# Kernel optimization log

Measured on AMD Instinct MI355X. Metric: run time of the kernel, lower is better.

## Reference

```python
import jax, jax.numpy as jnp
import numpy as np

B, N, G, K, V = 4, 512, 8, 64, 32000


def setup_inputs() -> dict:
    key = jax.random.key(0)
    k1, k2, k3 = jax.random.split(key, 3)
    phi = jax.random.normal(k1, (B, N, G, K), dtype=jnp.float32)
    # psi initialized uniform(-0.5, 0.5) as in torch.nn.init.uniform_
    psi = jax.random.uniform(k2, (V, K), dtype=jnp.float32, minval=-0.5, maxval=0.5)
    # perm[h, v] = index of h^{-1} acting on vocab word v (data-dependent permutation)
    perm = jax.random.randint(k3, (G, V), 0, V, dtype=jnp.int64)
    return {"phi": phi, "psi": psi, "perm": perm}


def reference(phi, psi, perm):
    # For each group element h: logits[b,n,v] += dot(phi[b,n,h,:], psi[perm[h,v],:])
    # Gather psi rows per group element: [G, V, K]
    psi_g = psi[perm]
    logits = jnp.einsum("bnhk,hvk->bnv", phi, psi_g)  # [B, N, V]
    return jax.nn.softmax(logits, axis=-1)
```

## Files before the change

### kernel.cpp

```cpp
#include <hip/hip_runtime.h>
#include <math.h>


#define M_ROWS 2048
#define V_DIM  32000
#define C_DIM  512
#define G_DIM  8
#define K_DIM  64
#define BM     128
#define BV     128
#define BK     32
#define NVBLK  (V_DIM / BV)
#define LDS_ROW 40

typedef _Float16 f16x8 __attribute__((ext_vector_type(8)));
typedef _Float16 f16x4 __attribute__((ext_vector_type(4)));
typedef float    f32x4 __attribute__((ext_vector_type(4)));

__global__ __launch_bounds__(256, 2) void gdecode_gemm(
    const float* __restrict__ phi, const float* __restrict__ psi,
    const int* __restrict__ perm, const int pstride,
    float* __restrict__ out, float* __restrict__ smax, float* __restrict__ ssum)
{
  __shared__ __align__(16) _Float16 lds[3 * BM * LDS_ROW];
  _Float16* sAhi = lds;
  _Float16* sAlo = lds + BM * LDS_ROW;
  _Float16* sB   = lds + 2 * BM * LDS_ROW;

  const int t     = threadIdx.x;
  const int vbase = blockIdx.x * BV;
  const int mbase = blockIdx.y * BM;

  const int kg = t & 7;
  const int r0 = t >> 3;

  const int wid  = t >> 6;
  const int lane = t & 63;
  const int wm   = wid & 1;
  const int wv   = wid >> 1;
  const int lrow = lane & 15;
  const int quad = lane >> 4;

  f32x4 acc[4][4] = {};

  for (int it = 0; it < 16; ++it) {
    const int cb  = it * BK;
    const int h   = cb >> 6;
    const int kin = cb & 63;

    float4 av[4], bv[4];
    #pragma unroll
    for (int i = 0; i < 4; ++i) {
      int m = r0 + i * 32;
      av[i] = *(const float4*)(phi + (size_t)(mbase + m) * C_DIM + cb + kg * 4);
    }
    #pragma unroll
    for (int i = 0; i < 4; ++i) {
      int v  = r0 + i * 32;
      int pr = perm[(size_t)(h * V_DIM + vbase + v) * pstride];
      bv[i]  = *(const float4*)(psi + (size_t)pr * K_DIM + kin + kg * 4);
    }

    __syncthreads();

    #pragma unroll
    for (int i = 0; i < 4; ++i) {
      int m = r0 + i * 32;
      float4 x = av[i];
      _Float16 h0 = (_Float16)x.x, h1 = (_Float16)x.y,
               h2 = (_Float16)x.z, h3 = (_Float16)x.w;
      f16x4 hi = {h0, h1, h2, h3};
      f16x4 lo = {(_Float16)(x.x - (float)h0), (_Float16)(x.y - (float)h1),
                  (_Float16)(x.z - (float)h2), (_Float16)(x.w - (float)h3)};
      *(f16x4*)(sAhi + m * LDS_ROW + kg * 4) = hi;
      *(f16x4*)(sAlo + m * LDS_ROW + kg * 4) = lo;
    }
    #pragma unroll
    for (int i = 0; i < 4; ++i) {
      int v = r0 + i * 32;
      float4 x = bv[i];
      f16x4 w = {(_Float16)x.x, (_Float16)x.y, (_Float16)x.z, (_Float16)x.w};
      *(f16x4*)(sB + v * LDS_ROW + kg * 4) = w;
    }

    __syncthreads();

    f16x8 ah[4], al[4], bf[4];
    #pragma unroll
    for (int i = 0; i < 4; ++i) {
      ah[i] = *(const f16x8*)(sAhi + (wm * 64 + i * 16 + lrow) * LDS_ROW + quad * 8);
      al[i] = *(const f16x8*)(sAlo + (wm * 64 + i * 16 + lrow) * LDS_ROW + quad * 8);
      bf[i] = *(const f16x8*)(sB   + (wv * 64 + i * 16 + lrow) * LDS_ROW + quad * 8);
    }
    #pragma unroll
    for (int i = 0; i < 4; ++i) {
      #pragma unroll
      for (int j = 0; j < 4; ++j) {
        acc[i][j] = __builtin_amdgcn_mfma_f32_16x16x32_f16(ah[i], bf[j], acc[i][j], 0, 0, 0);
        acc[i][j] = __builtin_amdgcn_mfma_f32_16x16x32_f16(al[i], bf[j], acc[i][j], 0, 0, 0);
      }
    }
  }

  __syncthreads();
  float* redmax = (float*)lds;
  float* redsum = redmax + 2 * BM;
  const int rowb = wm * 64;

  #pragma unroll
  for (int i = 0; i < 4; ++i) {
    #pragma unroll
    for (int r = 0; r < 4; ++r) {
      float v = fmaxf(fmaxf(acc[i][0][r], acc[i][1][r]),
                      fmaxf(acc[i][2][r], acc[i][3][r]));
      v = fmaxf(v, __shfl_xor(v, 1));
      v = fmaxf(v, __shfl_xor(v, 2));
      v = fmaxf(v, __shfl_xor(v, 4));
      v = fmaxf(v, __shfl_xor(v, 8));
      if (lrow == 0) redmax[(rowb + i * 16 + quad * 4 + r) * 2 + wv] = v;
    }
  }
  __syncthreads();
  float gmx[4][4];
  #pragma unroll
  for (int i = 0; i < 4; ++i) {
    #pragma unroll
    for (int r = 0; r < 4; ++r) {
      int row = rowb + i * 16 + quad * 4 + r;
      gmx[i][r] = fmaxf(redmax[row * 2], redmax[row * 2 + 1]);
    }
  }
  #pragma unroll
  for (int i = 0; i < 4; ++i) {
    #pragma unroll
    for (int r = 0; r < 4; ++r) {
      float s = __expf(acc[i][0][r] - gmx[i][r]) + __expf(acc[i][1][r] - gmx[i][r])
              + __expf(acc[i][2][r] - gmx[i][r]) + __expf(acc[i][3][r] - gmx[i][r]);
      s += __shfl_xor(s, 1);
      s += __shfl_xor(s, 2);
      s += __shfl_xor(s, 4);
      s += __shfl_xor(s, 8);
      if (lrow == 0) redsum[(rowb + i * 16 + quad * 4 + r) * 2 + wv] = s;
    }
  }
  __syncthreads();
  if (smax != nullptr && t < BM) {
    int row = t;
    size_t o = (size_t)(mbase + row) * NVBLK + blockIdx.x;
    smax[o] = fmaxf(redmax[row * 2], redmax[row * 2 + 1]);
    ssum[o] = redsum[row * 2] + redsum[row * 2 + 1];
  }
  #pragma unroll
  for (int i = 0; i < 4; ++i) {
    #pragma unroll
    for (int j = 0; j < 4; ++j) {
      #pragma unroll
      for (int r = 0; r < 4; ++r) {
        int grow = mbase + rowb + i * 16 + quad * 4 + r;
        int gcol = vbase + wv * 64 + j * 16 + lrow;
        out[(size_t)grow * V_DIM + gcol] = acc[i][j][r];
      }
    }
  }
}

__global__ __launch_bounds__(256) void gdecode_softmax_ws(
    float* __restrict__ out, const float* __restrict__ smax, const float* __restrict__ ssum)
{
  __shared__ float sbuf[4];
  const int m = blockIdx.x;
  const int t = threadIdx.x;
  const float* rm = smax + (size_t)m * NVBLK;
  const float* rs = ssum + (size_t)m * NVBLK;

  float lm = -3.4e38f;
  for (int i = t; i < NVBLK; i += 256) lm = fmaxf(lm, rm[i]);
  for (int d = 1; d < 64; d <<= 1) lm = fmaxf(lm, __shfl_xor(lm, d));
  if ((t & 63) == 0) sbuf[t >> 6] = lm;
  __syncthreads();
  const float M = fmaxf(fmaxf(sbuf[0], sbuf[1]), fmaxf(sbuf[2], sbuf[3]));
  __syncthreads();

  float ls = 0.f;
  for (int i = t; i < NVBLK; i += 256) ls += rs[i] * __expf(rm[i] - M);
  for (int d = 1; d < 64; d <<= 1) ls += __shfl_xor(ls, d);
  if ((t & 63) == 0) sbuf[t >> 6] = ls;
  __syncthreads();
  const float inv = 1.f / (sbuf[0] + sbuf[1] + sbuf[2] + sbuf[3]);

  float4* row = (float4*)(out + (size_t)m * V_DIM);
  for (int i = t; i < V_DIM / 4; i += 256) {
    float4 x = row[i];
    x.x = __expf(x.x - M) * inv;
    x.y = __expf(x.y - M) * inv;
    x.z = __expf(x.z - M) * inv;
    x.w = __expf(x.w - M) * inv;
    row[i] = x;
  }
}

__global__ __launch_bounds__(256) void gdecode_softmax_nows(float* __restrict__ out)
{
  __shared__ float sbuf[4];
  const int m = blockIdx.x;
  const int t = threadIdx.x;
  float4* row = (float4*)(out + (size_t)m * V_DIM);

  float lm = -3.4e38f;
  for (int i = t; i < V_DIM / 4; i += 256) {
    float4 x = row[i];
    lm = fmaxf(lm, fmaxf(fmaxf(x.x, x.y), fmaxf(x.z, x.w)));
  }
  for (int d = 1; d < 64; d <<= 1) lm = fmaxf(lm, __shfl_xor(lm, d));
  if ((t & 63) == 0) sbuf[t >> 6] = lm;
  __syncthreads();
  const float M = fmaxf(fmaxf(sbuf[0], sbuf[1]), fmaxf(sbuf[2], sbuf[3]));
  __syncthreads();

  float ls = 0.f;
  for (int i = t; i < V_DIM / 4; i += 256) {
    float4 x = row[i];
    ls += __expf(x.x - M) + __expf(x.y - M) + __expf(x.z - M) + __expf(x.w - M);
  }
  for (int d = 1; d < 64; d <<= 1) ls += __shfl_xor(ls, d);
  if ((t & 63) == 0) sbuf[t >> 6] = ls;
  __syncthreads();
  const float inv = 1.f / (sbuf[0] + sbuf[1] + sbuf[2] + sbuf[3]);

  for (int i = t; i < V_DIM / 4; i += 256) {
    float4 x = row[i];
    x.x = __expf(x.x - M) * inv;
    x.y = __expf(x.y - M) * inv;
    x.z = __expf(x.z - M) * inv;
    x.w = __expf(x.w - M) * inv;
    row[i] = x;
  }
}

extern "C" void kernel_launch(void* const* d_in, const int* in_sizes, int n_in,
                              void* d_out, int out_size, void* d_ws, size_t ws_size,
                              hipStream_t stream)
{
  const float* phi  = (const float*)d_in[0];
  const float* psi  = (const float*)d_in[1];
  const int*   perm = (const int*)d_in[2];
  const int pstride = (in_sizes[2] == 2 * G_DIM * V_DIM) ? 2 : 1;

  float* out = (float*)d_out;

  const size_t need = (size_t)M_ROWS * NVBLK * 2 * sizeof(float);
  const bool hasws = (d_ws != nullptr) && (ws_size >= need);
  float* smax = hasws ? (float*)d_ws : nullptr;
  float* ssum = hasws ? smax + (size_t)M_ROWS * NVBLK : nullptr;

  dim3 grid(NVBLK, M_ROWS / BM);
  gdecode_gemm<<<grid, 256, 0, stream>>>(phi, psi, perm, pstride, out, smax, ssum);

  if (hasws)
    gdecode_softmax_ws<<<M_ROWS, 256, 0, stream>>>(out, smax, ssum);
  else
    gdecode_softmax_nows<<<M_ROWS, 256, 0, stream>>>(out);
}
```

Before: 543.0 us.

## Pre-convert operands to fp16 tiles and stream them via global_load_lds

Adds prep kernels that split phi into hi/lo fp16 and gather plus convert psi rows into a tile-contiguous workspace layout. The GEMM then loads tiles directly into LDS with global_load_lds, with no per-iteration gather or conversion, and runs at higher occupancy. Softmax statistics are transposed, combined by a separate per-row kernel, and normalization uses nontemporal loads and stores across more blocks. This removes repeated gather and conversion work across M tiles, at the cost of extra launches and workspace traffic.

```diff
diff --git a/kernel.cpp b/kernel.cpp
--- a/kernel.cpp
+++ b/kernel.cpp
@@ -11,13 +11,220 @@
 #define BV     128
 #define BK     32
 #define NVBLK  (V_DIM / BV)
+#define NMT    (M_ROWS / BM)
+#define NKT    (C_DIM / BK)
 #define LDS_ROW 40
 
 typedef _Float16 f16x8 __attribute__((ext_vector_type(8)));
 typedef _Float16 f16x4 __attribute__((ext_vector_type(4)));
 typedef float    f32x4 __attribute__((ext_vector_type(4)));
 
-__global__ __launch_bounds__(256, 2) void gdecode_gemm(
+
+__device__ __forceinline__ void gl_lds16(const void* g, void* l) {
+  __builtin_amdgcn_global_load_lds(
+      (const __attribute__((address_space(1))) unsigned int*)g,
+      (__attribute__((address_space(3))) unsigned int*)l, 16, 0, 0);
+}
+
+__global__ __launch_bounds__(256) void gdecode_prep_phi(
+    const float* __restrict__ phi, _Float16* __restrict__ aws)
+{
+  const int ga   = blockIdx.x * 256 + threadIdx.x;
+  const int g    = ga & 511;
+  const int half = (ga >> 9) & 1;
+  const int tile = ga >> 10;
+  const int kq = g >> 7, r = g & 127;
+  const int m  = (tile >> 4) * BM + r;
+  const int k  = (tile & 15) * BK + kq * 8;
+  const float4 x0 = *(const float4*)(phi + (size_t)m * C_DIM + k);
+  const float4 x1 = *(const float4*)(phi + (size_t)m * C_DIM + k + 4);
+  const float xs[8] = {x0.x, x0.y, x0.z, x0.w, x1.x, x1.y, x1.z, x1.w};
+  f16x8 o;
+  #pragma unroll
+  for (int j = 0; j < 8; ++j) {
+    _Float16 hi = (_Float16)xs[j];
+    o[j] = half ? (_Float16)(xs[j] - (float)hi) : hi;
+  }
+  *(f16x8*)(aws + (size_t)ga * 8) = o;
+}
+
+__global__ __launch_bounds__(256) void gdecode_prep_psi(
+    const float* __restrict__ psi, const int* __restrict__ perm, const int pstride,
+    _Float16* __restrict__ bws)
+{
+  const int gb   = blockIdx.x * 256 + threadIdx.x;
+  const int g    = gb & 511;
+  const int tile = gb >> 9;
+  const int it = tile / 250;
+  const int vb = tile - it * 250;
+  const int kq = g >> 7, r = g & 127;
+  const int h   = it >> 1;
+  const int kin = (it & 1) * 32 + kq * 8;
+  const int v   = vb * BV + r;
+  const int pr  = perm[(size_t)(h * V_DIM + v) * pstride];
+  const float4 x0 = *(const float4*)(psi + (size_t)pr * K_DIM + kin);
+  const float4 x1 = *(const float4*)(psi + (size_t)pr * K_DIM + kin + 4);
+  f16x8 o = {(_Float16)x0.x, (_Float16)x0.y, (_Float16)x0.z, (_Float16)x0.w,
+             (_Float16)x1.x, (_Float16)x1.y, (_Float16)x1.z, (_Float16)x1.w};
+  *(f16x8*)(bws + (size_t)gb * 8) = o;
+}
+
+__global__ __launch_bounds__(256, 4) void gdecode_gemm2(
+    const _Float16* __restrict__ aws, const _Float16* __restrict__ bws,
+    float* __restrict__ out, float* __restrict__ smax, float* __restrict__ ssum)
+{
+  __shared__ __align__(16) _Float16 lds[3 * 4096];
+  _Float16* sAh = lds;
+  _Float16* sAl = lds + 4096;
+  _Float16* sB  = lds + 8192;
+
+  const int t  = threadIdx.x;
+  const int vb = blockIdx.x;
+  const int mt = blockIdx.y;
+  const int vbase = vb * BV;
+  const int mbase = mt * BM;
+
+  const int wid  = t >> 6;
+  const int lane = t & 63;
+  const int wm   = wid & 1;
+  const int wv   = wid >> 1;
+  const int lrow = lane & 15;
+  const int quad = lane >> 4;
+
+  const _Float16* gA = aws + (size_t)mt * NKT * 2 * 4096;
+  const _Float16* gB = bws + (size_t)vb * 4096;
+
+  f32x4 acc[4][4] = {};
+
+  for (int it = 0; it < 16; ++it) {
+    __syncthreads();
+    const _Float16* ga = gA + (size_t)it * 2 * 4096;
+    const _Float16* gb = gB + (size_t)it * NVBLK * 4096;
+    gl_lds16(ga + (size_t)t * 8,          sAh + t * 8);
+    gl_lds16(ga + 2048 + (size_t)t * 8,   sAh + 2048 + t * 8);
+    gl_lds16(ga + 4096 + (size_t)t * 8,   sAl + t * 8);
+    gl_lds16(ga + 6144 + (size_t)t * 8,   sAl + 2048 + t * 8);
+    gl_lds16(gb + (size_t)t * 8,          sB + t * 8);
+    gl_lds16(gb + 2048 + (size_t)t * 8,   sB + 2048 + t * 8);
+    __syncthreads();
+
+    f16x8 ah[4], al[4], bf[4];
+    #pragma unroll
+    for (int i = 0; i < 4; ++i) {
+      const int ra = quad * 1024 + (wm * 64 + i * 16 + lrow) * 8;
+      const int rb = quad * 1024 + (wv * 64 + i * 16 + lrow) * 8;
+      ah[i] = *(const f16x8*)(sAh + ra);
+      al[i] = *(const f16x8*)(sAl + ra);
+      bf[i] = *(const f16x8*)(sB + rb);
+    }
+    #pragma unroll
+    for (int i = 0; i < 4; ++i) {
+      #pragma unroll
+      for (int j = 0; j < 4; ++j) {
+        acc[i][j] = __builtin_amdgcn_mfma_f32_16x16x32_f16(ah[i], bf[j], acc[i][j], 0, 0, 0);
+        acc[i][j] = __builtin_amdgcn_mfma_f32_16x16x32_f16(al[i], bf[j], acc[i][j], 0, 0, 0);
+      }
+    }
+  }
+
+  __syncthreads();
+  float* redmax = (float*)lds;
+  float* redsum = redmax + 2 * BM;
+  const int rowb = wm * 64;
+
+  #pragma unroll
+  for (int i = 0; i < 4; ++i) {
+    #pragma unroll
+    for (int r = 0; r < 4; ++r) {
+      float v = fmaxf(fmaxf(acc[i][0][r], acc[i][1][r]),
+                      fmaxf(acc[i][2][r], acc[i][3][r]));
+      v = fmaxf(v, __shfl_xor(v, 1));
+      v = fmaxf(v, __shfl_xor(v, 2));
+      v = fmaxf(v, __shfl_xor(v, 4));
+      v = fmaxf(v, __shfl_xor(v, 8));
+      if (lrow == 0) redmax[(rowb + i * 16 + quad * 4 + r) * 2 + wv] = v;
+    }
+  }
+  __syncthreads();
+  float gmx[4][4];
+  #pragma unroll
+  for (int i = 0; i < 4; ++i) {
+    #pragma unroll
+    for (int r = 0; r < 4; ++r) {
+      int row = rowb + i * 16 + quad * 4 + r;
+      gmx[i][r] = fmaxf(redmax[row * 2], redmax[row * 2 + 1]);
+    }
+  }
+  #pragma unroll
+  for (int i = 0; i < 4; ++i) {
+    #pragma unroll
+    for (int r = 0; r < 4; ++r) {
+      float s = __expf(acc[i][0][r] - gmx[i][r]) + __expf(acc[i][1][r] - gmx[i][r])
+              + __expf(acc[i][2][r] - gmx[i][r]) + __expf(acc[i][3][r] - gmx[i][r]);
+      s += __shfl_xor(s, 1);
+      s += __shfl_xor(s, 2);
+      s += __shfl_xor(s, 4);
+      s += __shfl_xor(s, 8);
+      if (lrow == 0) redsum[(rowb + i * 16 + quad * 4 + r) * 2 + wv] = s;
+    }
+  }
+  __syncthreads();
+  if (t < BM) {
+    size_t o = (size_t)vb * M_ROWS + mbase + t;
+    smax[o] = fmaxf(redmax[t * 2], redmax[t * 2 + 1]);
+    ssum[o] = redsum[t * 2] + redsum[t * 2 + 1];
+  }
+  #pragma unroll
+  for (int i = 0; i < 4; ++i) {
+    #pragma unroll
+    for (int j = 0; j < 4; ++j) {
+      #pragma unroll
+      for (int r = 0; r < 4; ++r) {
+        int grow = mbase + rowb + i * 16 + quad * 4 + r;
+        int gcol = vbase + wv * 64 + j * 16 + lrow;
+        __builtin_nontemporal_store(acc[i][j][r], out + (size_t)grow * V_DIM + gcol);
+      }
+    }
+  }
+}
+
+__global__ __launch_bounds__(256) void gdecode_combine(
+    const float* __restrict__ smax, const float* __restrict__ ssum,
+    float* __restrict__ rowM, float* __restrict__ rowI)
+{
+  const int m = blockIdx.x * 256 + threadIdx.x;
+  float Mv = -3.4e38f;
+  #pragma unroll 5
+  for (int vb = 0; vb < NVBLK; ++vb) Mv = fmaxf(Mv, smax[(size_t)vb * M_ROWS + m]);
+  float S = 0.f;
+  #pragma unroll 5
+  for (int vb = 0; vb < NVBLK; ++vb)
+    S += ssum[(size_t)vb * M_ROWS + m] * __expf(smax[(size_t)vb * M_ROWS + m] - Mv);
+  rowM[m] = Mv;
+  rowI[m] = 1.f / S;
+}
+
+__global__ __launch_bounds__(256) void gdecode_norm(
+    float* __restrict__ out, const float* __restrict__ rowM, const float* __restrict__ rowI)
+{
+  const int m = blockIdx.x >> 2;
+  const int c = blockIdx.x & 3;
+  const float Mv = rowM[m];
+  const float Iv = rowI[m];
+  f32x4* row = (f32x4*)(out + (size_t)m * V_DIM + c * 8000);
+  for (int i = threadIdx.x; i < 2000; i += 256) {
+    f32x4 x = __builtin_nontemporal_load(row + i);
+    f32x4 y;
+    y[0] = __expf(x[0] - Mv) * Iv;
+    y[1] = __expf(x[1] - Mv) * Iv;
+    y[2] = __expf(x[2] - Mv) * Iv;
+    y[3] = __expf(x[3] - Mv) * Iv;
+    __builtin_nontemporal_store(y, row + i);
+  }
+}
+
+
+__global__ __launch_bounds__(256, 2) void gdecode_gemm_fb(
     const float* __restrict__ phi, const float* __restrict__ psi,
     const int* __restrict__ perm, const int pstride,
     float* __restrict__ out, float* __restrict__ smax, float* __restrict__ ssum)
@@ -237,6 +444,7 @@
   }
 }
 
+
 extern "C" void kernel_launch(void* const* d_in, const int* in_sizes, int n_in,
                               void* d_out, int out_size, void* d_ws, size_t ws_size,
                               hipStream_t stream)
@@ -248,13 +456,39 @@
 
   float* out = (float*)d_out;
 
-  const size_t need = (size_t)M_ROWS * NVBLK * 2 * sizeof(float);
-  const bool hasws = (d_ws != nullptr) && (ws_size >= need);
+  const size_t AWS_B  = (size_t)NMT * NKT * 2 * 4096 * 2;
+  const size_t BWS_B  = (size_t)NKT * NVBLK * 4096 * 2;
+  const size_t STAT_B = (size_t)NVBLK * M_ROWS * 4;
+  const size_t ROW_B  = (size_t)M_ROWS * 4;
+  const size_t need_fast = AWS_B + BWS_B + 2 * STAT_B + 2 * ROW_B;
+
+  if (d_ws != nullptr && ws_size >= need_fast) {
+    char* wp = (char*)d_ws;
+    _Float16* aws = (_Float16*)wp;                 wp += AWS_B;
+    _Float16* bws = (_Float16*)wp;                 wp += BWS_B;
+    float* smax   = (float*)wp;                    wp += STAT_B;
+    float* ssum   = (float*)wp;                    wp += STAT_B;
+    float* rowM   = (float*)wp;                    wp += ROW_B;
+    float* rowI   = (float*)wp;
+
+    gdecode_prep_phi<<<(NMT * NKT * 2 * 512) / 256, 256, 0, stream>>>(phi, aws);
+    gdecode_prep_psi<<<(NKT * NVBLK * 512) / 256, 256, 0, stream>>>(psi, perm, pstride, bws);
+
+    dim3 grid(NVBLK, NMT);
+    gdecode_gemm2<<<grid, 256, 0, stream>>>(aws, bws, out, smax, ssum);
+
+    gdecode_combine<<<M_ROWS / 256, 256, 0, stream>>>(smax, ssum, rowM, rowI);
+    gdecode_norm<<<M_ROWS * 4, 256, 0, stream>>>(out, rowM, rowI);
+    return;
+  }
+
+  const size_t need_old = (size_t)M_ROWS * NVBLK * 2 * sizeof(float);
+  const bool hasws = (d_ws != nullptr) && (ws_size >= need_old);
   float* smax = hasws ? (float*)d_ws : nullptr;
   float* ssum = hasws ? smax + (size_t)M_ROWS * NVBLK : nullptr;
 
   dim3 grid(NVBLK, M_ROWS / BM);
-  gdecode_gemm<<<grid, 256, 0, stream>>>(phi, psi, perm, pstride, out, smax, ssum);
+  gdecode_gemm_fb<<<grid, 256, 0, stream>>>(phi, psi, perm, pstride, out, smax, ssum);
 
   if (hasws)
     gdecode_softmax_ws<<<M_ROWS, 256, 0, stream>>>(out, smax, ssum);
```

New measurement: 594.0 us. 9.4% more time.
